# Optimization experiments

Measured on AMD Instinct MI355X. Metric: run time of the kernel, lower is better.

Reference implementation:

```python
import jax, jax.numpy as jnp
import numpy as np

B, N, C, H = 8, 1025, 768, 12
HD = C // H  # 64
SCALE = HD ** -0.5


def rotate_half(x):
    x1, x2 = jnp.split(x, 2, axis=-1)
    return jnp.concatenate((-x2, x1), axis=-1)


def apply_rope(x, sin, cos):
    return x * cos + rotate_half(x) * sin


def setup_inputs() -> dict:
    key = jax.random.key(0)
    ks = jax.random.split(key, 7)
    x = jax.random.normal(ks[0], (B, N, C), dtype=jnp.float32)
    sin = jax.random.normal(ks[1], (N - 1, HD), dtype=jnp.float32)
    cos = jax.random.normal(ks[2], (N - 1, HD), dtype=jnp.float32)
    s = 1.0 / np.sqrt(C)
    qkv_w = jax.random.normal(ks[3], (3 * C, C), dtype=jnp.float32) * s
    qkv_b = jnp.zeros((3 * C,), dtype=jnp.float32)
    proj_w = jax.random.normal(ks[4], (C, C), dtype=jnp.float32) * s
    proj_b = jnp.zeros((C,), dtype=jnp.float32)
    return {"x": x, "sin": sin, "cos": cos, "qkv_w": qkv_w, "qkv_b": qkv_b,
            "proj_w": proj_w, "proj_b": proj_b}


def reference(x, sin, cos, qkv_w, qkv_b, proj_w, proj_b):
    b, n, c = x.shape
    qkv = x @ qkv_w.T + qkv_b                      # [B,N,3C]
    qkv = qkv.reshape(b, n, 3, H, HD)
    qkv = jnp.transpose(qkv, (2, 0, 3, 1, 4))      # [3,B,H,N,HD]
    q, k, v = qkv[0], qkv[1], qkv[2]
    # RoPE on patch tokens only (cls token at index 0 excluded)
    q_patch = apply_rope(q[:, :, 1:, :], sin, cos)
    k_patch = apply_rope(k[:, :, 1:, :], sin, cos)
    q = jnp.concatenate((q[:, :, :1, :], q_patch), axis=2)
    k = jnp.concatenate((k[:, :, :1, :], k_patch), axis=2)
    attn = jnp.einsum('bhqd,bhkd->bhqk', q, k) * SCALE
    attn = jax.nn.softmax(attn, axis=-1)
    out = jnp.einsum('bhqk,bhkd->bhqd', attn, v)   # [B,H,N,HD]
    out = jnp.transpose(out, (0, 2, 1, 3)).reshape(b, n, c)
    out = out @ proj_w.T + proj_b
    return out
```

## Files before the change

### kernel.cpp

```cpp
#include <hip/hip_runtime.h>
#include <hip/hip_bf16.h>

constexpr int NTOK   = 1025;
constexpr int M      = 8 * NTOK;
constexpr int MP     = 8320;
constexpr int KDIM   = 768;
constexpr int NQKV   = 2304;
constexpr int NKVPAD = 1088;
constexpr float SCALEL2 = 0.125f * 1.44269504f;

using bf16x8 = __attribute__((ext_vector_type(8))) short;
using f32x4  = __attribute__((ext_vector_type(4))) float;

__device__ __forceinline__ f32x4 mfma_bf16(bf16x8 a, bf16x8 b, f32x4 c) {
  return __builtin_amdgcn_mfma_f32_16x16x32_bf16(a, b, c, 0, 0, 0);
}

__device__ __forceinline__ void gl16(const void* g, void* l) {
  __builtin_amdgcn_global_load_lds(
      (const __attribute__((address_space(1))) void*)g,
      (__attribute__((address_space(3))) void*)l, 16, 0, 0);
}

template <int N> __device__ __forceinline__ void wait_vmcnt() {
  if constexpr (N == 0)
    asm volatile("s_waitcnt vmcnt(0)" ::: "memory");
  else if constexpr (N == 4)
    asm volatile("s_waitcnt vmcnt(4)" ::: "memory");
  else if constexpr (N == 6)
    asm volatile("s_waitcnt vmcnt(6)" ::: "memory");
}

__device__ __forceinline__ float exp2_raw(float x) {
  float r;
  asm("v_exp_f32 %0, %1" : "=v"(r) : "v"(x));
  return r;
}
__device__ __forceinline__ unsigned short cvt_bf16_u16(float x) {
  unsigned u;
  asm("v_cvt_pk_bf16_f32 %0, %1, %2" : "=v"(u) : "v"(x), "v"(x));
  return (unsigned short)(u & 0xffffu);
}
__device__ __forceinline__ __hip_bfloat16 cvt_bf16_raw(float x) {
  union { unsigned short s; __hip_bfloat16 b; } c;
  c.s = cvt_bf16_u16(x);
  return c.b;
}

constexpr size_t SZ_X     = (size_t)MP * KDIM * 2;
constexpr size_t SZ_WQ    = (size_t)NQKV * KDIM * 2;
constexpr size_t SZ_PW    = (size_t)KDIM * KDIM * 2;
constexpr size_t SZ_QK    = (size_t)96 * NTOK * 64 * 2;
constexpr size_t SZ_VT    = (size_t)96 * 64 * NKVPAD * 2;
constexpr size_t OFF_XHI  = 0;
constexpr size_t OFF_XLO  = OFF_XHI + SZ_X;
constexpr size_t OFF_WQHI = OFF_XLO + SZ_X;
constexpr size_t OFF_PWHI = OFF_WQHI + SZ_WQ;
constexpr size_t OFF_PWLO = OFF_PWHI + SZ_PW;
constexpr size_t OFF_Q    = OFF_PWLO + SZ_PW;
constexpr size_t OFF_K    = OFF_Q + SZ_QK;
constexpr size_t OFF_VT   = OFF_K + SZ_QK;
constexpr size_t OFF_AO   = OFF_VT + SZ_VT;

constexpr int N4_X  = MP * KDIM / 4;
constexpr int N4_WQ = NQKV * KDIM / 4;
constexpr int N4_PW = KDIM * KDIM / 4;
constexpr int NPADC = NKVPAD - NTOK;
constexpr int N4_PAD = 96 * 64 * NPADC / 4;
constexpr int N4_TOT = N4_X + N4_WQ + N4_PW + N4_PAD;

__global__ void k_prep(const float* __restrict__ x, const float* __restrict__ qkvw,
                       const float* __restrict__ projw,
                       __hip_bfloat16* __restrict__ xhi,
                       __hip_bfloat16* __restrict__ wqhi,
                       __hip_bfloat16* __restrict__ pwhi,
                       __hip_bfloat16* __restrict__ pwlo,
                       __hip_bfloat16* __restrict__ vt) {
  const int u = blockIdx.x * 256 + threadIdx.x;
  if (u < N4_X) {
    const int i = u * 4;
    ushort4 o = {0, 0, 0, 0};
    if (i < M * KDIM) {
      const float4 v = *(const float4*)(x + i);
      o = ushort4{cvt_bf16_u16(v.x), cvt_bf16_u16(v.y), cvt_bf16_u16(v.z),
                  cvt_bf16_u16(v.w)};
    }
    *(ushort4*)((unsigned short*)xhi + i) = o;
  } else if (u < N4_X + N4_WQ) {
    const int i = (u - N4_X) * 4;
    const float4 v = *(const float4*)(qkvw + i);
    *(ushort4*)((unsigned short*)wqhi + i) = ushort4{
        cvt_bf16_u16(v.x), cvt_bf16_u16(v.y), cvt_bf16_u16(v.z), cvt_bf16_u16(v.w)};
  } else if (u < N4_X + N4_WQ + N4_PW) {
    const int i = (u - N4_X - N4_WQ) * 4;
    const float4 v = *(const float4*)(projw + i);
    float vv[4] = {v.x, v.y, v.z, v.w};
    unsigned short h[4], l[4];
#pragma unroll
    for (int k = 0; k < 4; ++k) {
      h[k] = cvt_bf16_u16(vv[k]);
      union { unsigned ui; float f; } c;
      c.ui = (unsigned)h[k] << 16;
      l[k] = cvt_bf16_u16(vv[k] - c.f);
    }
    *(ushort4*)((unsigned short*)pwhi + i) = ushort4{h[0], h[1], h[2], h[3]};
    *(ushort4*)((unsigned short*)pwlo + i) = ushort4{l[0], l[1], l[2], l[3]};
  } else {
    const int e0 = (u - N4_X - N4_WQ - N4_PW) * 4;
#pragma unroll
    for (int k = 0; k < 4; ++k) {
      const int e = e0 + k;
      const int r = e / NPADC;
      const int c = NTOK + (e - r * NPADC);
      vt[(size_t)r * NKVPAD + c] = __float2bfloat16(0.0f);
    }
  }
}

template <int NBX>
__global__ __launch_bounds__(256) void k_gemm_qkv(
    const __hip_bfloat16* __restrict__ A, const __hip_bfloat16* __restrict__ B,
    const float* __restrict__ bias, const float* __restrict__ sinp,
    const float* __restrict__ cosp, __hip_bfloat16* __restrict__ o_q,
    __hip_bfloat16* __restrict__ o_k, __hip_bfloat16* __restrict__ o_vt) {
  const int tid = threadIdx.x;
  const int w = tid >> 6, lane = tid & 63;
  const int wm = w >> 1, wn = w & 1;
  const int l15 = lane & 15, q4 = lane >> 4;

  const int nwg = gridDim.x;
  const int orig = blockIdx.x;
  const int qc = nwg >> 3, rc = nwg & 7;
  const int xcd = orig & 7, o8 = orig >> 3;
  const int wg =
      (xcd < rc ? xcd * (qc + 1) : rc * (qc + 1) + (xcd - rc) * qc) + o8;
  const int bx = wg % NBX, by = wg / NBX;
  const int mBase = by * 128, nBase = bx * 128;

  __shared__ __hip_bfloat16 sm[2][2][128 * 64];
  const char* pA = (const char*)A + (size_t)mBase * 1536;
  const char* pB = (const char*)B + (size_t)nBase * 1536;

  int stSrc[4], stDst[4];
#pragma unroll
  for (int i = 0; i < 4; ++i) {
    const int c = i * 256 + tid;
    const int row = c >> 3;
    stSrc[i] = row * 1536 + (((c & 7) ^ (row & 7)) << 4);
    stDst[i] = c << 4;
  }
  auto stage = [&](int kt, int buf) {
    const int kofs = kt * 128;
#pragma unroll
    for (int i = 0; i < 4; ++i) {
      gl16(pA + stSrc[i] + kofs, (char*)&sm[buf][0][0] + stDst[i]);
      gl16(pB + stSrc[i] + kofs, (char*)&sm[buf][1][0] + stDst[i]);
    }
  };

  int fA[2][4], fB[2][4];
#pragma unroll
  for (int f = 0; f < 4; ++f) {
    const int ra = wm * 64 + f * 16 + l15;
    const int rb = wn * 64 + f * 16 + l15;
#pragma unroll
    for (int ks = 0; ks < 2; ++ks) {
      fA[ks][f] = ra * 128 + (((ks * 4 + q4) ^ (ra & 7)) << 4);
      fB[ks][f] = rb * 128 + (((ks * 4 + q4) ^ (rb & 7)) << 4);
    }
  }

  f32x4 acc[4][4] = {};

  stage(0, 0);
  __syncthreads();

  for (int kt = 0; kt < 12; ++kt) {
    const int cur = kt & 1;
    if (kt < 11) stage(kt + 1, cur ^ 1);
    const char* sA = (const char*)&sm[cur][0][0];
    const char* sB = (const char*)&sm[cur][1][0];
    bf16x8 a[2][4], b[2][4];
#pragma unroll
    for (int ks = 0; ks < 2; ++ks)
#pragma unroll
      for (int f = 0; f < 4; ++f) {
        a[ks][f] = *(const bf16x8*)(sA + fA[ks][f]);
        b[ks][f] = *(const bf16x8*)(sB + fB[ks][f]);
      }
    __builtin_amdgcn_s_setprio(1);
#pragma unroll
    for (int mt = 0; mt < 4; ++mt)
#pragma unroll
      for (int nt = 0; nt < 4; ++nt) {
        acc[mt][nt] = mfma_bf16(a[0][mt], b[0][nt], acc[mt][nt]);
        acc[mt][nt] = mfma_bf16(a[1][mt], b[1][nt], acc[mt][nt]);
      }
    __builtin_amdgcn_s_setprio(0);
    __syncthreads();
  }

#pragma unroll
  for (int mt = 0; mt < 4; ++mt)
#pragma unroll
    for (int j = 0; j < 4; ++j) {
      const int gm = mBase + wm * 64 + mt * 16 + q4 * 4 + j;
      if (gm >= M) continue;
      const int b = gm / NTOK;
      const int t = gm - b * NTOK;
#pragma unroll
      for (int nt = 0; nt < 4; ++nt) {
        const int gc = nBase + wn * 64 + nt * 16 + l15;
        float v = acc[mt][nt][j] + bias[gc];
        const int three = gc / 768;
        const int hd = gc - three * 768;
        const int h = hd >> 6, d = hd & 63;
        const int bh = b * 12 + h;
        if (three == 2) {
          o_vt[((size_t)bh * 64 + d) * NKVPAD + t] = __float2bfloat16(v);
        } else {
          if (t > 0) {
            const float pv = acc[mt][nt ^ 2][j] + bias[gc ^ 32];
            const int so = (t - 1) * 64 + d;
            v = v * cosp[so] + ((d < 32) ? -pv : pv) * sinp[so];
          }
          if (three == 0)
            o_q[((size_t)bh * NTOK + t) * 64 + d] = __float2bfloat16(v);
          else
            o_k[((size_t)bh * NTOK + t) * 64 + d] = __float2bfloat16(v * SCALEL2);
        }
      }
    }
}

template <int NBX>
__global__ __launch_bounds__(256) void k_gemm_proj(
    const __hip_bfloat16* __restrict__ Ahi, const __hip_bfloat16* __restrict__ Asec,
    const __hip_bfloat16* __restrict__ Bhi, const float* __restrict__ bias,
    float* __restrict__ o_f32) {
  const int tid = threadIdx.x;
  const int w = tid >> 6, lane = tid & 63;
  const int wm = w >> 1, wn = w & 1;
  const int l15 = lane & 15, q4 = lane >> 4;

  const int nwg = gridDim.x;
  const int orig = blockIdx.x;
  const int qc = nwg >> 3, rc = nwg & 7;
  const int xcd = orig & 7, o8 = orig >> 3;
  const int wg =
      (xcd < rc ? xcd * (qc + 1) : rc * (qc + 1) + (xcd - rc) * qc) + o8;
  const int bx = wg % NBX, by = wg / NBX;
  const int mBase = by * 128, nBase = bx * 128;

  __shared__ __hip_bfloat16 sm[3][3 * 4096];

  const char* p0 = (const char*)Ahi + (size_t)mBase * (KDIM * 2);
  const char* p1 = (const char*)Asec + (size_t)nBase * (KDIM * 2);
  const char* p2 = (const char*)Bhi + (size_t)nBase * (KDIM * 2);

  const int slog = ((tid & 3) ^ ((tid >> 3) & 3)) << 4;
  const int ph = ((q4 ^ ((l15 >> 1) & 3)) << 4);

  auto stage = [&](int kt, int buf) {
    const int kofs = kt * 64;
    char* base = (char*)sm[buf];
#pragma unroll
    for (int i = 0; i < 2; ++i) {
      const int c = i * 256 + tid;
      const size_t rb = (size_t)(i * 64 + (tid >> 2)) * (KDIM * 2) + slog + kofs;
      gl16(p0 + rb, base + (size_t)c * 16);
      gl16(p1 + rb, base + 8192 + (size_t)c * 16);
      gl16(p2 + rb, base + 16384 + (size_t)c * 16);
    }
  };

  f32x4 acc[4][4] = {};

  stage(0, 0);
  stage(1, 1);

  constexpr int NKT = KDIM / 32;
  for (int kt = 0; kt < NKT; ++kt) {
    if (kt < NKT - 1)
      wait_vmcnt<6>();
    else
      wait_vmcnt<0>();
    __builtin_amdgcn_s_barrier();
    if (kt + 2 < NKT) stage(kt + 2, (kt + 2) % 3);
    char* s0 = (char*)sm[kt % 3];
    char* s1 = s0 + 8192;
    char* s2 = s0 + 16384;
    bf16x8 a0[4], b0[4], b1[4];
#pragma unroll
    for (int mt = 0; mt < 4; ++mt) {
      const int r = wm * 64 + mt * 16 + l15;
      a0[mt] = *(const bf16x8*)(s0 + r * 64 + ph);
    }
#pragma unroll
    for (int nt = 0; nt < 4; ++nt) {
      const int r = wn * 64 + nt * 16 + l15;
      b0[nt] = *(const bf16x8*)(s2 + r * 64 + ph);
      b1[nt] = *(const bf16x8*)(s1 + r * 64 + ph);
    }
    __builtin_amdgcn_s_setprio(1);
#pragma unroll
    for (int mt = 0; mt < 4; ++mt)
#pragma unroll
      for (int nt = 0; nt < 4; ++nt) {
        acc[mt][nt] = mfma_bf16(a0[mt], b0[nt], acc[mt][nt]);
        acc[mt][nt] = mfma_bf16(a0[mt], b1[nt], acc[mt][nt]);
      }
    __builtin_amdgcn_s_setprio(0);
  }

#pragma unroll
  for (int mt = 0; mt < 4; ++mt)
#pragma unroll
    for (int j = 0; j < 4; ++j) {
      const int gm = mBase + wm * 64 + mt * 16 + q4 * 4 + j;
      if (gm >= M) continue;
#pragma unroll
      for (int nt = 0; nt < 4; ++nt) {
        const int gc = nBase + wn * 64 + nt * 16 + l15;
        o_f32[(size_t)gm * 768 + gc] = acc[mt][nt][j] + bias[gc];
      }
    }
}

__global__ __launch_bounds__(256) void k_attn(
    const __hip_bfloat16* __restrict__ Q, const __hip_bfloat16* __restrict__ Kk,
    const __hip_bfloat16* __restrict__ VT, __hip_bfloat16* __restrict__ ao) {
  __shared__ __hip_bfloat16 Kt[3][64 * 64];
  __shared__ __hip_bfloat16 Vt[3][64 * 64];
  __shared__ __hip_bfloat16 Pl[4][32][72];
  const int tid = threadIdx.x, w = tid >> 6, lane = tid & 63;
  const int l15 = lane & 15, q4 = lane >> 4;
  const int id = blockIdx.x;
  const int xcd = id & 7, sub = id >> 3;
  const int hh = sub / 9;
  const int bh = xcd * 12 + hh;
  const int qb = (sub - hh * 9) * 128 + w * 32;
  const size_t qbase = (size_t)bh * NTOK * 64;
  const char* Kb = (const char*)(Kk + qbase);
  const char* Vb = (const char*)(VT + (size_t)bh * 64 * NKVPAD);

  int frag_off[2][4];
#pragma unroll
  for (int f = 0; f < 4; ++f) {
    const int row = f * 16 + l15;
#pragma unroll
    for (int ks = 0; ks < 2; ++ks)
      frag_off[ks][f] = row * 128 + (((ks * 4 + q4) ^ (row & 7)) << 4);
  }
  int stRow[2], sch16[2], stK[2], stV[2], ldsOff[2];
#pragma unroll
  for (int i = 0; i < 2; ++i) {
    const int c = i * 256 + tid;
    const int row = c >> 3;
    stRow[i] = row;
    sch16[i] = ((c & 7) ^ (row & 7)) << 4;
    stK[i] = row * 128 + sch16[i];
    stV[i] = row * (NKVPAD * 2) + sch16[i];
    ldsOff[i] = c * 16;
  }
  int pw_off[2][4], pa_off[2][2];
#pragma unroll
  for (int mt = 0; mt < 2; ++mt) {
#pragma unroll
    for (int j = 0; j < 4; ++j)
      pw_off[mt][j] = ((w * 32 + mt * 16 + q4 * 4 + j) * 72 + l15) * 2;
#pragma unroll
    for (int ks = 0; ks < 2; ++ks)
      pa_off[mt][ks] = ((w * 32 + mt * 16 + l15) * 72 + ks * 32 + q4 * 8) * 2;
  }
  char* Plc = (char*)&Pl[0][0][0];

  bf16x8 qa[2][2];
#pragma unroll
  for (int mt = 0; mt < 2; ++mt) {
    int t = qb + mt * 16 + l15;
    if (t > NTOK - 1) t = NTOK - 1;
#pragma unroll
    for (int ks = 0; ks < 2; ++ks)
      qa[mt][ks] = *(const bf16x8*)(Q + qbase + (size_t)t * 64 + ks * 32 + q4 * 8);
  }

  f32x4 accO[2][4] = {};
  float mrun[2][4], lpart[2][4];
#pragma unroll
  for (int mt = 0; mt < 2; ++mt)
#pragma unroll
    for (int j = 0; j < 4; ++j) {
      mrun[mt][j] = -1e30f;
      lpart[mt][j] = 0.0f;
    }

  auto stageKV = [&](int kt, int b) {
    const int kb0 = kt * 64;
#pragma unroll
    for (int i = 0; i < 2; ++i) {
      const char* srcK;
      if (kt == 16) {
        const int srow = min(kb0 + stRow[i], NTOK - 1);
        srcK = Kb + (size_t)srow * 128 + sch16[i];
      } else {
        srcK = Kb + (size_t)kb0 * 128 + stK[i];
      }
      gl16(srcK, (char*)&Kt[b][0] + ldsOff[i]);
      gl16(Vb + (size_t)kb0 * 2 + stV[i], (char*)&Vt[b][0] + ldsOff[i]);
    }
  };

  auto step = [&](int kt, int cur, bool last) {
    f32x4 s[2][4] = {};
    {
      const char* Kc = (const char*)&Kt[cur][0];
      bf16x8 kfr[2][4];
#pragma unroll
      for (int nt = 0; nt < 4; ++nt)
#pragma unroll
        for (int ks = 0; ks < 2; ++ks)
          kfr[ks][nt] = *(const bf16x8*)(Kc + frag_off[ks][nt]);
      __builtin_amdgcn_s_setprio(1);
#pragma unroll
      for (int mt = 0; mt < 2; ++mt)
#pragma unroll
        for (int nt = 0; nt < 4; ++nt)
#pragma unroll
          for (int ks = 0; ks < 2; ++ks)
            s[mt][nt] = mfma_bf16(qa[mt][ks], kfr[ks][nt], s[mt][nt]);
      __builtin_amdgcn_s_setprio(0);
    }
    if (last) {
#pragma unroll
      for (int nt = 0; nt < 4; ++nt)
        if (1024 + nt * 16 + l15 > NTOK - 1) {
#pragma unroll
          for (int mt = 0; mt < 2; ++mt)
#pragma unroll
            for (int j = 0; j < 4; ++j) s[mt][nt][j] = -1e30f;
        }
    }
    float smax[2][4];
    bool okl = true;
#pragma unroll
    for (int mt = 0; mt < 2; ++mt)
#pragma unroll
      for (int j = 0; j < 4; ++j) {
        const float a =
            fmaxf(fmaxf(s[mt][0][j], s[mt][1][j]), fmaxf(s[mt][2][j], s[mt][3][j]));
        smax[mt][j] = a;
        okl = okl && (a <= mrun[mt][j] + 8.0f);
      }
    if (!__all((int)okl)) {
#pragma unroll
      for (int mt = 0; mt < 2; ++mt)
#pragma unroll
        for (int j = 0; j < 4; ++j) {
          float m0 = smax[mt][j];
#pragma unroll
          for (int off = 1; off < 16; off <<= 1) m0 = fmaxf(m0, __shfl_xor(m0, off));
          const float mnew = fmaxf(mrun[mt][j], m0);
          const float fsc = exp2_raw(mrun[mt][j] - mnew);
          lpart[mt][j] *= fsc;
          mrun[mt][j] = mnew;
#pragma unroll
          for (int nd = 0; nd < 4; ++nd) accO[mt][nd][j] *= fsc;
        }
    }
#pragma unroll
    for (int mt = 0; mt < 2; ++mt)
#pragma unroll
      for (int j = 0; j < 4; ++j) {
        float acc = 0.0f;
        char* pw = Plc + pw_off[mt][j];
#pragma unroll
        for (int nt = 0; nt < 4; ++nt) {
          const float p = exp2_raw(s[mt][nt][j] - mrun[mt][j]);
          acc += p;
          *(__hip_bfloat16*)(pw + nt * 32) = cvt_bf16_raw(p);
        }
        lpart[mt][j] += acc;
      }
    bf16x8 pa[2][2], vf[2][4];
#pragma unroll
    for (int mt = 0; mt < 2; ++mt)
#pragma unroll
      for (int ks = 0; ks < 2; ++ks)
        pa[mt][ks] = *(const bf16x8*)(Plc + pa_off[mt][ks]);
    {
      const char* Vc = (const char*)&Vt[cur][0];
#pragma unroll
      for (int nd = 0; nd < 4; ++nd)
#pragma unroll
        for (int ks = 0; ks < 2; ++ks)
          vf[ks][nd] = *(const bf16x8*)(Vc + frag_off[ks][nd]);
    }
    __builtin_amdgcn_s_setprio(1);
#pragma unroll
    for (int mt = 0; mt < 2; ++mt)
#pragma unroll
      for (int nd = 0; nd < 4; ++nd)
#pragma unroll
        for (int ks = 0; ks < 2; ++ks)
          accO[mt][nd] = mfma_bf16(pa[mt][ks], vf[ks][nd], accO[mt][nd]);
    __builtin_amdgcn_s_setprio(0);
  };

  stageKV(0, 0);
  stageKV(1, 1);
  for (int kt = 0; kt < 17; ++kt) {
    if (kt < 16)
      wait_vmcnt<4>();
    else
      wait_vmcnt<0>();
    __builtin_amdgcn_s_barrier();
    if (kt + 2 < 17) stageKV(kt + 2, (kt + 2) % 3);
    step(kt, kt % 3, kt == 16);
  }

  const int b = bh / 12, h = bh - (bh / 12) * 12;
#pragma unroll
  for (int mt = 0; mt < 2; ++mt)
#pragma unroll
    for (int j = 0; j < 4; ++j) {
      float sum = lpart[mt][j];
#pragma unroll
      for (int off2 = 1; off2 < 16; off2 <<= 1) sum += __shfl_xor(sum, off2);
      const int t = qb + mt * 16 + q4 * 4 + j;
      if (t > NTOK - 1) continue;
      const float inv = 1.0f / sum;
      const size_t ro = ((size_t)(b * NTOK + t)) * 768 + h * 64;
#pragma unroll
      for (int nd = 0; nd < 4; ++nd) {
        const int d = nd * 16 + l15;
        ao[ro + d] = __float2bfloat16(accO[mt][nd][j] * inv);
      }
    }
}

extern "C" void kernel_launch(void* const* d_in, const int* in_sizes, int n_in,
                              void* d_out, int out_size, void* d_ws, size_t ws_size,
                              hipStream_t stream) {
  const float* x = (const float*)d_in[0];
  const float* sinp = (const float*)d_in[1];
  const float* cosp = (const float*)d_in[2];
  const float* qkvw = (const float*)d_in[3];
  const float* qkvb = (const float*)d_in[4];
  const float* projw = (const float*)d_in[5];
  const float* projb = (const float*)d_in[6];

  char* ws = (char*)d_ws;
  __hip_bfloat16* xhi = (__hip_bfloat16*)(ws + OFF_XHI);
  __hip_bfloat16* wqhi = (__hip_bfloat16*)(ws + OFF_WQHI);
  __hip_bfloat16* pwhi = (__hip_bfloat16*)(ws + OFF_PWHI);
  __hip_bfloat16* pwlo = (__hip_bfloat16*)(ws + OFF_PWLO);
  __hip_bfloat16* qb = (__hip_bfloat16*)(ws + OFF_Q);
  __hip_bfloat16* kb = (__hip_bfloat16*)(ws + OFF_K);
  __hip_bfloat16* vt = (__hip_bfloat16*)(ws + OFF_VT);
  __hip_bfloat16* ao = (__hip_bfloat16*)(ws + OFF_AO);

  k_prep<<<N4_TOT / 256, 256, 0, stream>>>(x, qkvw, projw, xhi, wqhi, pwhi, pwlo,
                                           vt);
  k_gemm_qkv<18><<<dim3(18 * 65), 256, 0, stream>>>(xhi, wqhi, qkvb, sinp, cosp,
                                                    qb, kb, vt);
  k_attn<<<dim3(864), 256, 0, stream>>>(qb, kb, vt, ao);
  k_gemm_proj<6><<<dim3(6 * 65), 256, 0, stream>>>(ao, pwlo, pwhi, projb,
                                                   (float*)d_out);
}
```

Measured before the change: 223.3 us.

## Enlarge QKV GEMM tile to 256x128 with 512 threads and 32-wide K steps

The QKV projection GEMM now uses 8 waves per block and a 256x128 output tile, halving the grid along M, while the K step per stage shrinks from 64 to 32 so the double-buffered LDS footprint stays moderate. The LDS swizzle is reworked for 64-byte rows, and the padded M is raised to a multiple of 256, which also changes the proj GEMM grid. The larger tile is meant to raise operand reuse per block and cut global traffic, but the shorter K steps double the loop trips and barriers, and fewer blocks may fill the GPU less evenly.

```diff
diff --git a/kernel.cpp b/kernel.cpp
--- a/kernel.cpp
+++ b/kernel.cpp
@@ -3,7 +3,7 @@
 
 constexpr int NTOK   = 1025;
 constexpr int M      = 8 * NTOK;
-constexpr int MP     = 8320;
+constexpr int MP     = 8448;
 constexpr int KDIM   = 768;
 constexpr int NQKV   = 2304;
 constexpr int NKVPAD = 1088;
@@ -53,8 +53,7 @@
 constexpr size_t SZ_QK    = (size_t)96 * NTOK * 64 * 2;
 constexpr size_t SZ_VT    = (size_t)96 * 64 * NKVPAD * 2;
 constexpr size_t OFF_XHI  = 0;
-constexpr size_t OFF_XLO  = OFF_XHI + SZ_X;
-constexpr size_t OFF_WQHI = OFF_XLO + SZ_X;
+constexpr size_t OFF_WQHI = OFF_XHI + SZ_X;
 constexpr size_t OFF_PWHI = OFF_WQHI + SZ_WQ;
 constexpr size_t OFF_PWLO = OFF_PWHI + SZ_PW;
 constexpr size_t OFF_Q    = OFF_PWLO + SZ_PW;
@@ -118,7 +117,7 @@
 }
 
 template <int NBX>
-__global__ __launch_bounds__(256) void k_gemm_qkv(
+__global__ __launch_bounds__(512) void k_gemm_qkv(
     const __hip_bfloat16* __restrict__ A, const __hip_bfloat16* __restrict__ B,
     const float* __restrict__ bias, const float* __restrict__ sinp,
     const float* __restrict__ cosp, __hip_bfloat16* __restrict__ o_q,
@@ -135,39 +134,43 @@
   const int wg =
       (xcd < rc ? xcd * (qc + 1) : rc * (qc + 1) + (xcd - rc) * qc) + o8;
   const int bx = wg % NBX, by = wg / NBX;
-  const int mBase = by * 128, nBase = bx * 128;
-
-  __shared__ __hip_bfloat16 sm[2][2][128 * 64];
+  const int mBase = by * 256, nBase = bx * 128;
+
+  __shared__ __hip_bfloat16 sm[2][12288];
+  constexpr int OFFB = 16384;
+
   const char* pA = (const char*)A + (size_t)mBase * 1536;
   const char* pB = (const char*)B + (size_t)nBase * 1536;
 
-  int stSrc[4], stDst[4];
-#pragma unroll
-  for (int i = 0; i < 4; ++i) {
-    const int c = i * 256 + tid;
-    const int row = c >> 3;
-    stSrc[i] = row * 1536 + (((c & 7) ^ (row & 7)) << 4);
-    stDst[i] = c << 4;
+  int sA_src[2], sA_dst[2], sB_src, sB_dst;
+#pragma unroll
+  for (int i = 0; i < 2; ++i) {
+    const int c = i * 512 + tid;
+    const int row = c >> 2;
+    sA_src[i] = row * 1536 + (((c & 3) ^ ((row >> 1) & 3)) << 4);
+    sA_dst[i] = c << 4;
+  }
+  {
+    const int c = tid;
+    const int row = c >> 2;
+    sB_src = row * 1536 + (((c & 3) ^ ((row >> 1) & 3)) << 4);
+    sB_dst = c << 4;
   }
   auto stage = [&](int kt, int buf) {
-    const int kofs = kt * 128;
-#pragma unroll
-    for (int i = 0; i < 4; ++i) {
-      gl16(pA + stSrc[i] + kofs, (char*)&sm[buf][0][0] + stDst[i]);
-      gl16(pB + stSrc[i] + kofs, (char*)&sm[buf][1][0] + stDst[i]);
-    }
+    const int kofs = kt * 64;
+    char* base = (char*)&sm[buf][0];
+#pragma unroll
+    for (int i = 0; i < 2; ++i) gl16(pA + sA_src[i] + kofs, base + sA_dst[i]);
+    gl16(pB + sB_src + kofs, base + OFFB + sB_dst);
   };
 
-  int fA[2][4], fB[2][4];
+  int fA[4], fB[4];
 #pragma unroll
   for (int f = 0; f < 4; ++f) {
     const int ra = wm * 64 + f * 16 + l15;
     const int rb = wn * 64 + f * 16 + l15;
-#pragma unroll
-    for (int ks = 0; ks < 2; ++ks) {
-      fA[ks][f] = ra * 128 + (((ks * 4 + q4) ^ (ra & 7)) << 4);
-      fB[ks][f] = rb * 128 + (((ks * 4 + q4) ^ (rb & 7)) << 4);
-    }
+    fA[f] = ra * 64 + ((q4 ^ ((ra >> 1) & 3)) << 4);
+    fB[f] = OFFB + rb * 64 + ((q4 ^ ((rb >> 1) & 3)) << 4);
   }
 
   f32x4 acc[4][4] = {};
@@ -175,27 +178,23 @@
   stage(0, 0);
   __syncthreads();
 
-  for (int kt = 0; kt < 12; ++kt) {
+  constexpr int NKT = KDIM / 32;
+  for (int kt = 0; kt < NKT; ++kt) {
     const int cur = kt & 1;
-    if (kt < 11) stage(kt + 1, cur ^ 1);
-    const char* sA = (const char*)&sm[cur][0][0];
-    const char* sB = (const char*)&sm[cur][1][0];
-    bf16x8 a[2][4], b[2][4];
-#pragma unroll
-    for (int ks = 0; ks < 2; ++ks)
-#pragma unroll
-      for (int f = 0; f < 4; ++f) {
-        a[ks][f] = *(const bf16x8*)(sA + fA[ks][f]);
-        b[ks][f] = *(const bf16x8*)(sB + fB[ks][f]);
-      }
+    if (kt + 1 < NKT) stage(kt + 1, cur ^ 1);
+    const char* s = (const char*)&sm[cur][0];
+    bf16x8 a[4], b[4];
+#pragma unroll
+    for (int f = 0; f < 4; ++f) {
+      a[f] = *(const bf16x8*)(s + fA[f]);
+      b[f] = *(const bf16x8*)(s + fB[f]);
+    }
     __builtin_amdgcn_s_setprio(1);
 #pragma unroll
     for (int mt = 0; mt < 4; ++mt)
 #pragma unroll
-      for (int nt = 0; nt < 4; ++nt) {
-        acc[mt][nt] = mfma_bf16(a[0][mt], b[0][nt], acc[mt][nt]);
-        acc[mt][nt] = mfma_bf16(a[1][mt], b[1][nt], acc[mt][nt]);
-      }
+      for (int nt = 0; nt < 4; ++nt)
+        acc[mt][nt] = mfma_bf16(a[mt], b[nt], acc[mt][nt]);
     __builtin_amdgcn_s_setprio(0);
     __syncthreads();
   }
@@ -562,9 +561,9 @@
 
   k_prep<<<N4_TOT / 256, 256, 0, stream>>>(x, qkvw, projw, xhi, wqhi, pwhi, pwlo,
                                            vt);
-  k_gemm_qkv<18><<<dim3(18 * 65), 256, 0, stream>>>(xhi, wqhi, qkvb, sinp, cosp,
+  k_gemm_qkv<18><<<dim3(18 * 33), 512, 0, stream>>>(xhi, wqhi, qkvb, sinp, cosp,
                                                     qb, kb, vt);
   k_attn<<<dim3(864), 256, 0, stream>>>(qb, kb, vt, ao);
-  k_gemm_proj<6><<<dim3(6 * 65), 256, 0, stream>>>(ao, pwlo, pwhi, projb,
+  k_gemm_proj<6><<<dim3(6 * 66), 256, 0, stream>>>(ao, pwlo, pwhi, projb,
                                                    (float*)d_out);
 }
```

After: 235.6 us. +5.5%, slower.
